# Kernel tuning notes

Measured on AMD Instinct MI355X. Metric: run time of the kernel, lower is better.

The kernel has to match this reference:

```python
import jax, jax.numpy as jnp
import numpy as np
from jax import lax


def _layernorm(x, g, b, eps=1e-5):
    m = x.mean(-1, keepdims=True)
    v = ((x - m) ** 2).mean(-1, keepdims=True)
    return (x - m) * lax.rsqrt(v + eps) * g + b


def _conv1d(x, w, b):
    # x: (B, T, Cin), w: (K, Cin, Cout) -> SAME padding (kernel=3, pad=1)
    y = lax.conv_general_dilated(x, w, (1,), 'SAME',
                                 dimension_numbers=('NWC', 'WIO', 'NWC'))
    return y + b


def _predictor(x, params, mask):
    w1, b1, g1, be1, w2, b2, g2, be2, wl, bl = params
    h = _layernorm(jax.nn.relu(_conv1d(x, w1, b1)), g1, be1)
    h = _layernorm(jax.nn.relu(_conv1d(h, w2, b2)), g2, be2)
    out = (h @ wl)[..., 0] + bl[0]          # (B, T)
    return jnp.where(mask, 0.0, out)


def _length_regulate(x, dur, max_len):
    # vectorized equivalent of the per-token expand/cat/pad loop
    cum = jnp.cumsum(dur, axis=1)            # (B, S)
    mel_len = cum[:, -1]                     # (B,)
    pos = jnp.arange(max_len)                # (T,)
    idx = jax.vmap(lambda c: jnp.searchsorted(c, pos, side='right'))(cum)
    idx = jnp.minimum(idx, x.shape[1] - 1)   # (B, T)
    out = jnp.take_along_axis(x, idx[:, :, None], axis=1)
    valid = (pos[None, :] < mel_len[:, None])[:, :, None]
    return jnp.where(valid, out, 0.0), mel_len


def setup_inputs() -> dict:
    key = jax.random.key(0)
    ks = jax.random.split(key, 12)
    B, S, D, F, K, T, NB = 32, 512, 512, 512, 3, 4096, 256
    inp = {
        'x': jax.random.normal(ks[0], (B, S, D), jnp.float32),
        'src_mask': jnp.zeros((B, S), bool),
        'mel_mask': jnp.zeros((B, T), bool),
        'pitch_truth': jax.random.normal(ks[1], (B, S), jnp.float32),
        'energy_truth': jax.random.normal(ks[2], (B, S), jnp.float32),
        'duration_truth': jax.random.randint(ks[3], (B, S), 0, 8, jnp.int32),
        'conv1_w': 0.05 * jax.random.normal(ks[4], (3, K, D, F), jnp.float32),
        'conv1_b': jnp.zeros((3, F), jnp.float32),
        'ln1_g': jnp.ones((3, F), jnp.float32),
        'ln1_b': jnp.zeros((3, F), jnp.float32),
        'conv2_w': 0.05 * jax.random.normal(ks[5], (3, K, F, F), jnp.float32),
        'conv2_b': jnp.zeros((3, F), jnp.float32),
        'ln2_g': jnp.ones((3, F), jnp.float32),
        'ln2_b': jnp.zeros((3, F), jnp.float32),
        'lin_w': 0.05 * jax.random.normal(ks[6], (3, F, 1), jnp.float32),
        'lin_b': jnp.zeros((3, 1), jnp.float32),
        'pitch_emb': 0.05 * jax.random.normal(ks[7], (NB, D), jnp.float32),
        'energy_emb': 0.05 * jax.random.normal(ks[8], (NB, D), jnp.float32),
        'pitch_bins': jnp.linspace(-3.0, 3.0, NB - 1),
        'energy_bins': jnp.linspace(-3.0, 3.0, NB - 1),
        'max_mel_len': T,
    }
    return inp


def reference(x, src_mask, mel_mask, pitch_truth, energy_truth, duration_truth,
              conv1_w, conv1_b, ln1_g, ln1_b, conv2_w, conv2_b, ln2_g, ln2_b,
              lin_w, lin_b, pitch_emb, energy_emb, pitch_bins, energy_bins,
              max_mel_len):
    def params(i):
        return (conv1_w[i], conv1_b[i], ln1_g[i], ln1_b[i],
                conv2_w[i], conv2_b[i], ln2_g[i], ln2_b[i], lin_w[i], lin_b[i])

    # pitch (predictor idx 0)
    pitch_pred = _predictor(x, params(0), src_mask)
    x = x + pitch_emb[jnp.searchsorted(pitch_bins, pitch_truth, side='left')]
    # energy (idx 1)
    energy_pred = _predictor(x, params(1), src_mask)
    x = x + energy_emb[jnp.searchsorted(energy_bins, energy_truth, side='left')]
    # duration (idx 2)
    log_dur = _predictor(x, params(2), src_mask)
    # length regulation with ground-truth durations (training path)
    x_out, mel_len = _length_regulate(x, duration_truth, max_mel_len)
    return x_out, pitch_pred, energy_pred, log_dur, mel_len, mel_mask
```

## Files before the change

kernel.cpp:

```cpp
#include <hip/hip_runtime.h>
#include <hip/hip_bf16.h>


#define B_ 32
#define S_ 512
#define D_ 512
#define F_ 512
#define T_ 4096
#define SP_ 514
#define KK_ 1536
#define NKT 48
#define SLOT ((size_t)B_ * SP_ * D_)

typedef __attribute__((ext_vector_type(8))) short bf16x8;
typedef __attribute__((ext_vector_type(4))) float f32x4;

__device__ __forceinline__ float bf2f(unsigned short u) {
  union { unsigned int i; float f; } c; c.i = (unsigned int)u << 16; return c.f;
}
__device__ __forceinline__ unsigned short f2bf(float f) {
  __hip_bfloat16 h = __float2bfloat16(f);
  return *(unsigned short*)&h;
}

struct Job {
  const __hip_bfloat16* Pin;
  const __hip_bfloat16* WT;
  const float* bias;
  const float* g;
  const float* be;
  const float* wl;
  const float* bl;
  const unsigned char* mask;
  __hip_bfloat16* Pout;
  float* pred;
  int mode;
};

#define WT_BLKS 1152
#define TP_BLKS 8224
__global__ __launch_bounds__(256) void prep_k(const float* __restrict__ x,
                                              const float* __restrict__ W1,
                                              const float* __restrict__ W2,
                                              const int* __restrict__ dur,
                                              const float* __restrict__ ptruth,
                                              const float* __restrict__ pbins,
                                              const float* __restrict__ pemb,
                                              const float* __restrict__ etruth,
                                              const float* __restrict__ ebins,
                                              const float* __restrict__ eemb,
                                              __hip_bfloat16* __restrict__ X0,
                                              __hip_bfloat16* __restrict__ X1,
                                              __hip_bfloat16* __restrict__ X2,
                                              __hip_bfloat16* __restrict__ P0,
                                              __hip_bfloat16* __restrict__ P1,
                                              __hip_bfloat16* __restrict__ WT1,
                                              __hip_bfloat16* __restrict__ WT2,
                                              int* __restrict__ cum,
                                              float* __restrict__ mel_len) {
  const int blk = blockIdx.x;
  const int t = threadIdx.x;
  if (blk < WT_BLKS) {
    __shared__ float tb[64][65];
    const int w = blk / 192;
    const int kt = (blk % 192) >> 3;
    const int ft = blk & 7;
    const float* src = (w < 3) ? (W1 + (size_t)w * KK_ * F_)
                               : (W2 + (size_t)(w - 3) * KK_ * F_);
    __hip_bfloat16* dst = (w < 3) ? (WT1 + (size_t)w * KK_ * F_)
                                  : (WT2 + (size_t)(w - 3) * KK_ * F_);
    const int ty = t >> 4, tx = t & 15;
    #pragma unroll
    for (int j = 0; j < 4; ++j) {
      const int r = ty + j * 16;
      const float4 v = *(const float4*)(src + (size_t)(kt * 64 + r) * F_ + ft * 64 + tx * 4);
      tb[r][tx * 4 + 0] = v.x; tb[r][tx * 4 + 1] = v.y;
      tb[r][tx * 4 + 2] = v.z; tb[r][tx * 4 + 3] = v.w;
    }
    __syncthreads();
    #pragma unroll
    for (int j = 0; j < 4; ++j) {
      const int r = ty + j * 16;
      ushort4 u = make_ushort4(f2bf(tb[tx * 4 + 0][r]), f2bf(tb[tx * 4 + 1][r]),
                               f2bf(tb[tx * 4 + 2][r]), f2bf(tb[tx * 4 + 3][r]));
      *(ushort4*)((unsigned short*)dst + (size_t)(ft * 64 + r) * KK_ + kt * 64 + tx * 4) = u;
    }
  } else if (blk < WT_BLKS + TP_BLKS) {
    __shared__ int i1s[2], i2s[2];
    const int half = t >> 7;
    const int tl = t & 127;
    const int task = (blk - WT_BLKS) * 2 + half;
    if (task < B_ * S_) {
      if (tl == 0) {
        float v = ptruth[task];
        int lo = 0, hi = 255;
        while (lo < hi) { const int mid = (lo + hi) >> 1; if (pbins[mid] < v) lo = mid + 1; else hi = mid; }
        i1s[half] = lo;
        v = etruth[task]; lo = 0; hi = 255;
        while (lo < hi) { const int mid = (lo + hi) >> 1; if (ebins[mid] < v) lo = mid + 1; else hi = mid; }
        i2s[half] = lo;
      }
      __syncthreads();
      const int b = task >> 9, s = task & 511;
      const size_t off = ((size_t)b * SP_ + s + 1) * D_ + tl * 4;
      const float4 v = *(const float4*)(x + (size_t)task * D_ + tl * 4);
      const float4 pe = *(const float4*)(pemb + (size_t)i1s[half] * D_ + tl * 4);
      const float4 ee = *(const float4*)(eemb + (size_t)i2s[half] * D_ + tl * 4);
      *(ushort4*)((unsigned short*)X0 + off) =
          make_ushort4(f2bf(v.x), f2bf(v.y), f2bf(v.z), f2bf(v.w));
      const float4 v1 = make_float4(v.x + pe.x, v.y + pe.y, v.z + pe.z, v.w + pe.w);
      *(ushort4*)((unsigned short*)X1 + off) =
          make_ushort4(f2bf(v1.x), f2bf(v1.y), f2bf(v1.z), f2bf(v1.w));
      *(ushort4*)((unsigned short*)X2 + off) =
          make_ushort4(f2bf(v1.x + ee.x), f2bf(v1.y + ee.y),
                       f2bf(v1.z + ee.z), f2bf(v1.w + ee.w));
    } else {
      __syncthreads();
      const int idx = task - B_ * S_;
      const int b = idx >> 1;
      const int r = (idx & 1) ? (SP_ - 1) : 0;
      const size_t off = ((size_t)b * SP_ + r) * D_ + tl * 4;
      const ushort4 z = make_ushort4(0, 0, 0, 0);
      *(ushort4*)((unsigned short*)X0 + off) = z;
      *(ushort4*)((unsigned short*)X1 + off) = z;
      *(ushort4*)((unsigned short*)X2 + off) = z;
      *(ushort4*)((unsigned short*)P0 + off) = z;
      *(ushort4*)((unsigned short*)P1 + off) = z;
    }
  } else {
    __shared__ int sh[S_];
    const int b = blk - (WT_BLKS + TP_BLKS);
    sh[t] = dur[b * S_ + t];
    sh[t + 256] = dur[b * S_ + t + 256];
    __syncthreads();
    for (int off = 1; off < S_; off <<= 1) {
      const int a1 = (t >= off) ? sh[t - off] : 0;
      const int j2 = t + 256;
      const int a2 = (j2 >= off) ? sh[j2 - off] : 0;
      __syncthreads();
      sh[t] += a1; sh[j2] += a2;
      __syncthreads();
    }
    cum[b * S_ + t] = sh[t];
    cum[b * S_ + t + 256] = sh[t + 256];
    if (t == 255) mel_len[b] = (float)sh[S_ - 1];
  }
}

__global__ __launch_bounds__(512, 4) void convfuse_k(Job j0, Job j1, Job j2) {
  extern __shared__ char smem[];
  char* As = smem;
  char* Bs = smem + 2 * 4096;
  const int pid = blockIdx.x >> 8;
  const Job jb = (pid == 0) ? j0 : (pid == 1 ? j1 : j2);
  const int inner = blockIdx.x & 255;
  const int swz = (inner & 7) * 32 + (inner >> 3);
  const int b  = swz >> 3;
  const int st = (swz & 7) * 64;
  const int t = threadIdx.x;
  const int lane = t & 63;
  const int wave = t >> 6;
  const int wn = wave * 64;

  f32x4 acc[4][4];
  #pragma unroll
  for (int m = 0; m < 4; ++m)
    #pragma unroll
    for (int n = 0; n < 4; ++n) acc[m][n] = (f32x4){0.f, 0.f, 0.f, 0.f};

  const __hip_bfloat16* Xb = jb.Pin + (size_t)b * SP_ * D_;
  const __hip_bfloat16* WT = jb.WT;

  auto stage = [&](int kt, int buf) {
    char* Ad = As + buf * 4096;
    if (t < 256) {
      const int row = t >> 2, ch = t & 3;
      const __hip_bfloat16* ga = Xb + (size_t)(st + (kt >> 4) + row) * D_ +
                                 (kt & 15) * 32 + (ch ^ ((row >> 1) & 3)) * 8;
      __builtin_amdgcn_global_load_lds(
          (const __attribute__((address_space(1))) void*)ga,
          (__attribute__((address_space(3))) void*)(Ad + t * 16), 16, 0, 0);
    }
    char* Bd = Bs + buf * 32768;
    #pragma unroll
    for (int i = 0; i < 4; ++i) {
      const int c = t + i * 512;
      const int fr = c >> 2, ch = c & 3;
      const __hip_bfloat16* gb = WT + (size_t)fr * KK_ + kt * 32 +
                                 (ch ^ ((fr >> 1) & 3)) * 8;
      __builtin_amdgcn_global_load_lds(
          (const __attribute__((address_space(1))) void*)gb,
          (__attribute__((address_space(3))) void*)(Bd + c * 16), 16, 0, 0);
    }
  };

  stage(0, 0);
  __syncthreads();
  const int rA = lane & 15;
  const int offx = ((lane >> 4) * 16) ^ (((rA >> 1) & 3) << 4);

  for (int kt = 0; kt < NKT; ++kt) {
    const int cur = kt & 1;
    if (kt < NKT - 1) stage(kt + 1, cur ^ 1);
    const char* Ab = As + cur * 4096;
    const char* Bb = Bs + cur * 32768;
    bf16x8 af[4], bf[4];
    #pragma unroll
    for (int m = 0; m < 4; ++m)
      af[m] = *(const bf16x8*)(Ab + (m * 16 + rA) * 64 + offx);
    #pragma unroll
    for (int n = 0; n < 4; ++n)
      bf[n] = *(const bf16x8*)(Bb + (wn + n * 16 + rA) * 64 + offx);
    __builtin_amdgcn_s_setprio(1);
    #pragma unroll
    for (int m = 0; m < 4; ++m)
      #pragma unroll
      for (int n = 0; n < 4; ++n)
        acc[m][n] = __builtin_amdgcn_mfma_f32_16x16x32_bf16(af[m], bf[n], acc[m][n], 0, 0, 0);
    __builtin_amdgcn_s_setprio(0);
    __syncthreads();
  }

  float* rS = (float*)smem;
  float* rQ = rS + 512;
  float* rP = rQ + 512;
  float* tS = rP + 512;
  float* tQ = tS + 64;
  float* tP = tQ + 64;
  float* wG = tP + 64;
  float* wB = wG + 8;

  const int MODE = jb.mode;
  float bia[4], gg[4], bb[4], ww[4];
  #pragma unroll
  for (int n = 0; n < 4; ++n) {
    const int f = wn + n * 16 + rA;
    bia[n] = jb.bias[f]; gg[n] = jb.g[f]; bb[n] = jb.be[f];
    ww[n] = (MODE == 1) ? jb.wl[f] : 0.f;
  }
  if (MODE == 1) {
    float gwp = 0.f, bwp = 0.f;
    #pragma unroll
    for (int n = 0; n < 4; ++n) { gwp += gg[n] * ww[n]; bwp += bb[n] * ww[n]; }
    #pragma unroll
    for (int o = 1; o < 16; o <<= 1) {
      gwp += __shfl_xor(gwp, o); bwp += __shfl_xor(bwp, o);
    }
    if (lane == 0) { wG[wave] = gwp; wB[wave] = bwp; }
  }
  #pragma unroll
  for (int m = 0; m < 4; ++m) {
    #pragma unroll
    for (int r = 0; r < 4; ++r) {
      float sv = 0.f, sq = 0.f, sp = 0.f;
      #pragma unroll
      for (int n = 0; n < 4; ++n) {
        float v = fmaxf(acc[m][n][r] + bia[n], 0.f);
        acc[m][n][r] = v;
        sv += v; sq += v * v;
        sp += v * gg[n] * ww[n];
      }
      #pragma unroll
      for (int o = 1; o < 16; o <<= 1) {
        sv += __shfl_xor(sv, o); sq += __shfl_xor(sq, o);
        sp += __shfl_xor(sp, o);
      }
      if (rA == 0) {
        const int row = m * 16 + (lane >> 4) * 4 + r;
        rS[wave * 64 + row] = sv; rQ[wave * 64 + row] = sq;
        rP[wave * 64 + row] = sp;
      }
    }
  }
  __syncthreads();
  if (t < 64) {
    float S = 0.f, Q = 0.f, Pp = 0.f;
    #pragma unroll
    for (int w = 0; w < 8; ++w) {
      S += rS[w * 64 + t]; Q += rQ[w * 64 + t]; Pp += rP[w * 64 + t];
    }
    tS[t] = S; tQ[t] = Q; tP[t] = Pp;
  }
  __syncthreads();
  if (MODE == 0) {
    unsigned short* Pu = (unsigned short*)jb.Pout;
    #pragma unroll
    for (int m = 0; m < 4; ++m) {
      #pragma unroll
      for (int r = 0; r < 4; ++r) {
        const int row = m * 16 + (lane >> 4) * 4 + r;
        const float mean = tS[row] * (1.f / F_);
        const float var = tQ[row] * (1.f / F_) - mean * mean;
        const float inv = rsqrtf(var + 1e-5f);
        unsigned short* pp =
            Pu + ((size_t)b * SP_ + st + row + 1) * D_ + wn + rA;
        #pragma unroll
        for (int n = 0; n < 4; ++n)
          pp[n * 16] = f2bf((acc[m][n][r] - mean) * inv * gg[n] + bb[n]);
      }
    }
  } else {
    if (t < 64) {
      float GW = 0.f, BW = 0.f;
      #pragma unroll
      for (int w = 0; w < 8; ++w) { GW += wG[w]; BW += wB[w]; }
      const float mean = tS[t] * (1.f / F_);
      const float var = tQ[t] * (1.f / F_) - mean * mean;
      const float inv = rsqrtf(var + 1e-5f);
      const int grow = b * S_ + st + t;
      jb.pred[grow] = jb.mask[grow] ? 0.f
                                    : (inv * tP[t] - inv * mean * GW + BW + jb.bl[0]);
    }
  }
}

__global__ __launch_bounds__(256) void gather_k(const __hip_bfloat16* __restrict__ X,
                                                const int* __restrict__ cum,
                                                const unsigned char* __restrict__ melm,
                                                float* __restrict__ out,
                                                float* __restrict__ maskf) {
  const int b    = blockIdx.x >> 11;
  const int pos0 = (blockIdx.x & 2047) * 2;
  const int half = threadIdx.x >> 7;
  const int tl   = threadIdx.x & 127;
  const int pos  = pos0 + half;
  __shared__ int sidx[2], svalid[2];
  if (tl == 0) {
    const int* c = cum + b * S_;
    int lo = 0, hi = S_;
    while (lo < hi) {
      const int mid = (lo + hi) >> 1;
      if (c[mid] <= pos) lo = mid + 1; else hi = mid;
    }
    sidx[half] = (lo < S_ - 1) ? lo : (S_ - 1);
    svalid[half] = (pos < c[S_ - 1]) ? 1 : 0;
    maskf[(size_t)b * T_ + pos] = melm[(size_t)b * T_ + pos] ? 1.f : 0.f;
  }
  __syncthreads();
  float4 v = make_float4(0.f, 0.f, 0.f, 0.f);
  if (svalid[half]) {
    const ushort4 u = *(const ushort4*)((const unsigned short*)X +
                        ((size_t)b * SP_ + sidx[half] + 1) * D_ + tl * 4);
    v = make_float4(bf2f(u.x), bf2f(u.y), bf2f(u.z), bf2f(u.w));
  }
  *(float4*)(out + ((size_t)b * T_ + pos) * D_ + tl * 4) = v;
}

extern "C" void kernel_launch(void* const* d_in, const int* in_sizes, int n_in,
                              void* d_out, int out_size, void* d_ws, size_t ws_size,
                              hipStream_t stream) {
  const float* x            = (const float*)d_in[0];
  const unsigned char* srcm = (const unsigned char*)d_in[1];
  const unsigned char* melm = (const unsigned char*)d_in[2];
  const float* pitch_truth  = (const float*)d_in[3];
  const float* energy_truth = (const float*)d_in[4];
  const int*   dur          = (const int*)d_in[5];
  const float* conv1_w = (const float*)d_in[6];
  const float* conv1_b = (const float*)d_in[7];
  const float* ln1_g   = (const float*)d_in[8];
  const float* ln1_b   = (const float*)d_in[9];
  const float* conv2_w = (const float*)d_in[10];
  const float* conv2_b = (const float*)d_in[11];
  const float* ln2_g   = (const float*)d_in[12];
  const float* ln2_b   = (const float*)d_in[13];
  const float* lin_w   = (const float*)d_in[14];
  const float* lin_b   = (const float*)d_in[15];
  const float* pitch_emb   = (const float*)d_in[16];
  const float* energy_emb  = (const float*)d_in[17];
  const float* pitch_bins  = (const float*)d_in[18];
  const float* energy_bins = (const float*)d_in[19];

  float* out      = (float*)d_out;
  float* x_out    = out;
  float* p_pitch  = out + (size_t)B_ * T_ * D_;
  float* p_energy = p_pitch + B_ * S_;
  float* p_dur    = p_energy + B_ * S_;
  float* p_mellen = p_dur + B_ * S_;
  float* p_mask   = p_mellen + B_;

  __hip_bfloat16* S0  = (__hip_bfloat16*)d_ws;
  __hip_bfloat16* S1  = S0 + SLOT;
  __hip_bfloat16* S2  = S1 + SLOT;
  __hip_bfloat16* S3  = S2 + SLOT;
  __hip_bfloat16* S4  = S3 + SLOT;
  __hip_bfloat16* WT1 = S4 + SLOT;
  __hip_bfloat16* WT2 = WT1 + (size_t)3 * F_ * KK_;
  int*  cum = (int*)(WT2 + (size_t)3 * F_ * KK_);

  const dim3 blk512t(512), blk256(256);
  const int convLds = 2 * (4096 + 32768);
  hipFuncSetAttribute((const void*)convfuse_k,
                      hipFuncAttributeMaxDynamicSharedMemorySize, convLds);

  prep_k<<<dim3(WT_BLKS + TP_BLKS + B_), blk256, 0, stream>>>(
      x, conv1_w, conv2_w, dur, pitch_truth, pitch_bins, pitch_emb,
      energy_truth, energy_bins, energy_emb,
      S0, S1, S2, S3, S4, WT1, WT2, cum, p_mellen);

  auto c1 = [&](int i, const __hip_bfloat16* in, __hip_bfloat16* Pout) {
    return Job{in, WT1 + (size_t)i * F_ * KK_, conv1_b + (size_t)i * F_,
               ln1_g + (size_t)i * F_, ln1_b + (size_t)i * F_,
               nullptr, nullptr, nullptr, Pout, nullptr, 0};
  };
  auto c2 = [&](int i, const __hip_bfloat16* in, float* pred) {
    return Job{in, WT2 + (size_t)i * F_ * KK_, conv2_b + (size_t)i * F_,
               ln2_g + (size_t)i * F_, ln2_b + (size_t)i * F_,
               lin_w + (size_t)i * F_, lin_b + i, srcm, nullptr, pred, 1};
  };

  {
    Job a = c1(0, S0, S3), b = c1(1, S1, S4);
    convfuse_k<<<dim3(512), blk512t, convLds, stream>>>(a, b, b);
  }
  {
    Job a = c2(0, S3, p_pitch), b = c2(1, S4, p_energy), c = c1(2, S2, S0);
    convfuse_k<<<dim3(768), blk512t, convLds, stream>>>(a, b, c);
  }
  {
    Job a = c2(2, S0, p_dur);
    convfuse_k<<<dim3(256), blk512t, convLds, stream>>>(a, a, a);
  }

  gather_k<<<dim3(B_ * T_ / 2), blk256, 0, stream>>>(S2, cum, melm, x_out, p_mask);
}
```

Measured before the change: 379.3 us.

## Enlarge conv GEMM tile to 128x512 with 8-phase pipelined K loop

Replaces the 64-row by 512-column conv tile with a 128x512 tile split into quadrant phases. Each phase overlaps global-to-LDS loads of the next K slice with MFMA on the current one, using explicit vmcnt waits and barriers. It also rebalances the three launches so each runs two jobs of 128 blocks. The goal is more reuse of the weight tile per block and fewer synchronizations. In exchange, the 160KB LDS footprint and larger accumulator set lower occupancy, and with 256 blocks per launch there may be fewer blocks than CUs would like.

```diff
diff --git a/kernel.cpp b/kernel.cpp
--- a/kernel.cpp
+++ b/kernel.cpp
@@ -9,7 +9,7 @@
 #define T_ 4096
 #define SP_ 514
 #define KK_ 1536
-#define NKT 48
+#define NITER 12
 #define SLOT ((size_t)B_ * SP_ * D_)
 
 typedef __attribute__((ext_vector_type(8))) short bf16x8;
@@ -147,137 +147,181 @@
   }
 }
 
-__global__ __launch_bounds__(512, 4) void convfuse_k(Job j0, Job j1, Job j2) {
+#define GLOAD(gptr, loff) __builtin_amdgcn_global_load_lds(                    \
+    (const __attribute__((address_space(1))) void*)(gptr),                     \
+    (__attribute__((address_space(3))) void*)(smem + (loff)), 16, 0, 0)
+
+#define PHASE(D, AH, BH, STAGE_STMT, VM_STMT)                                  \
+  {                                                                            \
+    bf16x8 aR[2][2], bR[2][4];                                                 \
+    const char* Ab = smem + (D) * 16384 + (AH) * 8192;                         \
+    const char* Bb = smem + 32768 + (D) * 65536 + (BH) * 32768;                \
+    _Pragma("unroll")                                                          \
+    for (int kh = 0; kh < 2; ++kh) {                                           \
+      _Pragma("unroll")                                                        \
+      for (int mi = 0; mi < 2; ++mi) {                                         \
+        const int row = rowbase + 16 * mi;                                     \
+        aR[kh][mi] = *(const bf16x8*)(Ab + row * 128 +                         \
+                                      (((kh * 4 + l4) ^ (row & 7)) * 16));     \
+      }                                                                        \
+      _Pragma("unroll")                                                        \
+      for (int ni = 0; ni < 4; ++ni) {                                         \
+        const int cl = colbase + 16 * ni;                                      \
+        bR[kh][ni] = *(const bf16x8*)(Bb + cl * 128 +                          \
+                                      (((kh * 4 + l4) ^ (cl & 7)) * 16));      \
+      }                                                                        \
+    }                                                                          \
+    STAGE_STMT;                                                                \
+    __builtin_amdgcn_s_barrier();                                              \
+    asm volatile("s_waitcnt lgkmcnt(0)" ::: "memory");                         \
+    __builtin_amdgcn_sched_barrier(0);                                         \
+    __builtin_amdgcn_s_setprio(1);                                             \
+    _Pragma("unroll")                                                          \
+    for (int kh = 0; kh < 2; ++kh)                                             \
+      _Pragma("unroll")                                                        \
+      for (int mi = 0; mi < 2; ++mi)                                           \
+        _Pragma("unroll")                                                      \
+        for (int ni = 0; ni < 4; ++ni)                                         \
+          acc[AH][BH][mi][ni] = __builtin_amdgcn_mfma_f32_16x16x32_bf16(       \
+              aR[kh][mi], bR[kh][ni], acc[AH][BH][mi][ni], 0, 0, 0);           \
+    __builtin_amdgcn_s_setprio(0);                                             \
+    __builtin_amdgcn_sched_barrier(0);                                         \
+    VM_STMT;                                                                   \
+    __builtin_amdgcn_s_barrier();                                              \
+  }
+
+__global__ __launch_bounds__(512, 2) void conv8_k(Job j0, Job j1) {
   extern __shared__ char smem[];
-  char* As = smem;
-  char* Bs = smem + 2 * 4096;
-  const int pid = blockIdx.x >> 8;
-  const Job jb = (pid == 0) ? j0 : (pid == 1 ? j1 : j2);
-  const int inner = blockIdx.x & 255;
-  const int swz = (inner & 7) * 32 + (inner >> 3);
-  const int b  = swz >> 3;
-  const int st = (swz & 7) * 64;
+  const Job jb = (blockIdx.x >> 7) ? j1 : j0;
+  const int inner = blockIdx.x & 127;
+  const int swz = (inner & 7) * 16 + (inner >> 3);
+  const int b  = swz >> 2;
+  const int st = (swz & 3) * 128;
   const int t = threadIdx.x;
   const int lane = t & 63;
   const int wave = t >> 6;
-  const int wn = wave * 64;
-
-  f32x4 acc[4][4];
+  const int wm2 = wave >> 2;
+  const int wn  = wave & 3;
+  const int rA = lane & 15;
+  const int l4 = lane >> 4;
+  const int rowbase = 32 * wm2 + rA;
+  const int colbase = 64 * wn + rA;
+
+  f32x4 acc[2][2][2][4];
   #pragma unroll
-  for (int m = 0; m < 4; ++m)
-    #pragma unroll
-    for (int n = 0; n < 4; ++n) acc[m][n] = (f32x4){0.f, 0.f, 0.f, 0.f};
-
-  const __hip_bfloat16* Xb = jb.Pin + (size_t)b * SP_ * D_;
-  const __hip_bfloat16* WT = jb.WT;
-
-  auto stage = [&](int kt, int buf) {
-    char* Ad = As + buf * 4096;
-    if (t < 256) {
-      const int row = t >> 2, ch = t & 3;
-      const __hip_bfloat16* ga = Xb + (size_t)(st + (kt >> 4) + row) * D_ +
-                                 (kt & 15) * 32 + (ch ^ ((row >> 1) & 3)) * 8;
-      __builtin_amdgcn_global_load_lds(
-          (const __attribute__((address_space(1))) void*)ga,
-          (__attribute__((address_space(3))) void*)(Ad + t * 16), 16, 0, 0);
-    }
-    char* Bd = Bs + buf * 32768;
+  for (int a = 0; a < 2; ++a)
+    #pragma unroll
+    for (int c = 0; c < 2; ++c)
+      #pragma unroll
+      for (int m = 0; m < 2; ++m)
+        #pragma unroll
+        for (int n = 0; n < 4; ++n) acc[a][c][m][n] = (f32x4){0.f, 0.f, 0.f, 0.f};
+
+  auto stageA = [&](int kt, int half) {
+    const int r = t >> 3, ch = t & 7;
+    const __hip_bfloat16* ga = jb.Pin +
+        ((size_t)b * SP_ + st + half * 64 + r + (kt >> 3)) * D_ +
+        (kt & 7) * 64 + (ch ^ (r & 7)) * 8;
+    GLOAD(ga, (kt & 1) * 16384 + half * 8192 + t * 16);
+  };
+  auto stageB = [&](int kt, int half) {
     #pragma unroll
     for (int i = 0; i < 4; ++i) {
       const int c = t + i * 512;
-      const int fr = c >> 2, ch = c & 3;
-      const __hip_bfloat16* gb = WT + (size_t)fr * KK_ + kt * 32 +
-                                 (ch ^ ((fr >> 1) & 3)) * 8;
-      __builtin_amdgcn_global_load_lds(
-          (const __attribute__((address_space(1))) void*)gb,
-          (__attribute__((address_space(3))) void*)(Bd + c * 16), 16, 0, 0);
+      const int fr = c >> 3, ch = c & 7;
+      const __hip_bfloat16* gb = jb.WT +
+          (size_t)(half * 256 + fr) * KK_ + kt * 64 + (ch ^ (fr & 7)) * 8;
+      GLOAD(gb, 32768 + (kt & 1) * 65536 + half * 32768 + c * 16);
     }
   };
 
-  stage(0, 0);
-  __syncthreads();
-  const int rA = lane & 15;
-  const int offx = ((lane >> 4) * 16) ^ (((rA >> 1) & 3) << 4);
-
-  for (int kt = 0; kt < NKT; ++kt) {
-    const int cur = kt & 1;
-    if (kt < NKT - 1) stage(kt + 1, cur ^ 1);
-    const char* Ab = As + cur * 4096;
-    const char* Bb = Bs + cur * 32768;
-    bf16x8 af[4], bf[4];
-    #pragma unroll
-    for (int m = 0; m < 4; ++m)
-      af[m] = *(const bf16x8*)(Ab + (m * 16 + rA) * 64 + offx);
-    #pragma unroll
-    for (int n = 0; n < 4; ++n)
-      bf[n] = *(const bf16x8*)(Bb + (wn + n * 16 + rA) * 64 + offx);
-    __builtin_amdgcn_s_setprio(1);
-    #pragma unroll
-    for (int m = 0; m < 4; ++m)
-      #pragma unroll
-      for (int n = 0; n < 4; ++n)
-        acc[m][n] = __builtin_amdgcn_mfma_f32_16x16x32_bf16(af[m], bf[n], acc[m][n], 0, 0, 0);
-    __builtin_amdgcn_s_setprio(0);
-    __syncthreads();
+  stageA(0, 0); stageB(0, 0); stageA(0, 1); stageB(0, 1);
+  stageA(1, 0); stageB(1, 1);
+  asm volatile("s_waitcnt vmcnt(5)" ::: "memory");
+  __builtin_amdgcn_s_barrier();
+
+  for (int it = 0; it < NITER; ++it) {
+    const int tk = 2 * it;
+    const bool more = (it < NITER - 1);
+    PHASE(0, 0, 0, { stageB(tk + 1, 0); }, );
+    PHASE(0, 0, 1, { stageA(tk + 1, 1); }, );
+    PHASE(0, 1, 1, { if (more) stageA(tk + 2, 0); }, );
+    PHASE(0, 1, 0, { if (more) stageB(tk + 2, 1); },
+          if (more) { asm volatile("s_waitcnt vmcnt(5)" ::: "memory"); }
+          else      { asm volatile("s_waitcnt vmcnt(0)" ::: "memory"); });
+    PHASE(1, 0, 0, { if (more) stageB(tk + 2, 0); }, );
+    PHASE(1, 0, 1, { if (more) stageA(tk + 2, 1); }, );
+    PHASE(1, 1, 1, { if (more) stageA(tk + 3, 0); }, );
+    PHASE(1, 1, 0, { if (more) stageB(tk + 3, 1); },
+          if (more) { asm volatile("s_waitcnt vmcnt(5)" ::: "memory"); }
+          else      { asm volatile("s_waitcnt vmcnt(0)" ::: "memory"); });
   }
 
   float* rS = (float*)smem;
   float* rQ = rS + 512;
   float* rP = rQ + 512;
   float* tS = rP + 512;
-  float* tQ = tS + 64;
-  float* tP = tQ + 64;
-  float* wG = tP + 64;
-  float* wB = wG + 8;
+  float* tQ = tS + 128;
+  float* tP = tQ + 128;
+  float* wG = tP + 128;
+  float* wB = wG + 4;
 
   const int MODE = jb.mode;
-  float bia[4], gg[4], bb[4], ww[4];
+  float bia[2][4], gg[2][4], bb[2][4], ww[2][4];
   #pragma unroll
-  for (int n = 0; n < 4; ++n) {
-    const int f = wn + n * 16 + rA;
-    bia[n] = jb.bias[f]; gg[n] = jb.g[f]; bb[n] = jb.be[f];
-    ww[n] = (MODE == 1) ? jb.wl[f] : 0.f;
-  }
-  if (MODE == 1) {
+  for (int bh = 0; bh < 2; ++bh)
+    #pragma unroll
+    for (int ni = 0; ni < 4; ++ni) {
+      const int f = 64 * wn + bh * 256 + 16 * ni + rA;
+      bia[bh][ni] = jb.bias[f]; gg[bh][ni] = jb.g[f]; bb[bh][ni] = jb.be[f];
+      ww[bh][ni] = (MODE == 1) ? jb.wl[f] : 0.f;
+    }
+  if (MODE == 1 && wm2 == 0) {
     float gwp = 0.f, bwp = 0.f;
     #pragma unroll
-    for (int n = 0; n < 4; ++n) { gwp += gg[n] * ww[n]; bwp += bb[n] * ww[n]; }
+    for (int bh = 0; bh < 2; ++bh)
+      #pragma unroll
+      for (int ni = 0; ni < 4; ++ni) {
+        gwp += gg[bh][ni] * ww[bh][ni]; bwp += bb[bh][ni] * ww[bh][ni];
+      }
     #pragma unroll
     for (int o = 1; o < 16; o <<= 1) {
       gwp += __shfl_xor(gwp, o); bwp += __shfl_xor(bwp, o);
     }
-    if (lane == 0) { wG[wave] = gwp; wB[wave] = bwp; }
+    if (lane == 0) { wG[wn] = gwp; wB[wn] = bwp; }
   }
   #pragma unroll
-  for (int m = 0; m < 4; ++m) {
-    #pragma unroll
-    for (int r = 0; r < 4; ++r) {
-      float sv = 0.f, sq = 0.f, sp = 0.f;
+  for (int ah = 0; ah < 2; ++ah)
+    #pragma unroll
+    for (int mi = 0; mi < 2; ++mi)
       #pragma unroll
-      for (int n = 0; n < 4; ++n) {
-        float v = fmaxf(acc[m][n][r] + bia[n], 0.f);
-        acc[m][n][r] = v;
-        sv += v; sq += v * v;
-        sp += v * gg[n] * ww[n];
+      for (int reg = 0; reg < 4; ++reg) {
+        float sv = 0.f, sq = 0.f, sp = 0.f;
+        #pragma unroll
+        for (int bh = 0; bh < 2; ++bh)
+          #pragma unroll
+          for (int ni = 0; ni < 4; ++ni) {
+            float v = fmaxf(acc[ah][bh][mi][ni][reg] + bia[bh][ni], 0.f);
+            acc[ah][bh][mi][ni][reg] = v;
+            sv += v; sq += v * v;
+            sp += v * gg[bh][ni] * ww[bh][ni];
+          }
+        #pragma unroll
+        for (int o = 1; o < 16; o <<= 1) {
+          sv += __shfl_xor(sv, o); sq += __shfl_xor(sq, o);
+          sp += __shfl_xor(sp, o);
+        }
+        if (rA == 0) {
+          const int lr = 64 * ah + 32 * wm2 + 16 * mi + l4 * 4 + reg;
+          rS[wn * 128 + lr] = sv; rQ[wn * 128 + lr] = sq; rP[wn * 128 + lr] = sp;
+        }
       }
-      #pragma unroll
-      for (int o = 1; o < 16; o <<= 1) {
-        sv += __shfl_xor(sv, o); sq += __shfl_xor(sq, o);
-        sp += __shfl_xor(sp, o);
-      }
-      if (rA == 0) {
-        const int row = m * 16 + (lane >> 4) * 4 + r;
-        rS[wave * 64 + row] = sv; rQ[wave * 64 + row] = sq;
-        rP[wave * 64 + row] = sp;
-      }
-    }
-  }
   __syncthreads();
-  if (t < 64) {
+  if (t < 128) {
     float S = 0.f, Q = 0.f, Pp = 0.f;
     #pragma unroll
-    for (int w = 0; w < 8; ++w) {
-      S += rS[w * 64 + t]; Q += rQ[w * 64 + t]; Pp += rP[w * 64 + t];
+    for (int w = 0; w < 4; ++w) {
+      S += rS[w * 128 + t]; Q += rQ[w * 128 + t]; Pp += rP[w * 128 + t];
     }
     tS[t] = S; tQ[t] = Q; tP[t] = Pp;
   }
@@ -285,25 +329,27 @@
   if (MODE == 0) {
     unsigned short* Pu = (unsigned short*)jb.Pout;
     #pragma unroll
-    for (int m = 0; m < 4; ++m) {
+    for (int ah = 0; ah < 2; ++ah)
       #pragma unroll
-      for (int r = 0; r < 4; ++r) {
-        const int row = m * 16 + (lane >> 4) * 4 + r;
-        const float mean = tS[row] * (1.f / F_);
-        const float var = tQ[row] * (1.f / F_) - mean * mean;
-        const float inv = rsqrtf(var + 1e-5f);
-        unsigned short* pp =
-            Pu + ((size_t)b * SP_ + st + row + 1) * D_ + wn + rA;
+      for (int mi = 0; mi < 2; ++mi)
         #pragma unroll
-        for (int n = 0; n < 4; ++n)
-          pp[n * 16] = f2bf((acc[m][n][r] - mean) * inv * gg[n] + bb[n]);
-      }
-    }
+        for (int reg = 0; reg < 4; ++reg) {
+          const int lr = 64 * ah + 32 * wm2 + 16 * mi + l4 * 4 + reg;
+          const float mean = tS[lr] * (1.f / F_);
+          const float var = tQ[lr] * (1.f / F_) - mean * mean;
+          const float inv = rsqrtf(var + 1e-5f);
+          unsigned short* pp = Pu + ((size_t)b * SP_ + st + lr + 1) * D_;
+          #pragma unroll
+          for (int bh = 0; bh < 2; ++bh)
+            #pragma unroll
+            for (int ni = 0; ni < 4; ++ni)
+              pp[64 * wn + bh * 256 + 16 * ni + rA] =
+                  f2bf((acc[ah][bh][mi][ni][reg] - mean) * inv * gg[bh][ni] + bb[bh][ni]);
+        }
   } else {
-    if (t < 64) {
-      float GW = 0.f, BW = 0.f;
-      #pragma unroll
-      for (int w = 0; w < 8; ++w) { GW += wG[w]; BW += wB[w]; }
+    if (t < 128) {
+      const float GW = wG[0] + wG[1] + wG[2] + wG[3];
+      const float BW = wB[0] + wB[1] + wB[2] + wB[3];
       const float mean = tS[t] * (1.f / F_);
       const float var = tQ[t] * (1.f / F_) - mean * mean;
       const float inv = rsqrtf(var + 1e-5f);
@@ -388,8 +434,8 @@
   int*  cum = (int*)(WT2 + (size_t)3 * F_ * KK_);
 
   const dim3 blk512t(512), blk256(256);
-  const int convLds = 2 * (4096 + 32768);
-  hipFuncSetAttribute((const void*)convfuse_k,
+  const int convLds = 163840;
+  hipFuncSetAttribute((const void*)conv8_k,
                       hipFuncAttributeMaxDynamicSharedMemorySize, convLds);
 
   prep_k<<<dim3(WT_BLKS + TP_BLKS + B_), blk256, 0, stream>>>(
@@ -410,15 +456,15 @@
 
   {
     Job a = c1(0, S0, S3), b = c1(1, S1, S4);
-    convfuse_k<<<dim3(512), blk512t, convLds, stream>>>(a, b, b);
+    conv8_k<<<dim3(256), blk512t, convLds, stream>>>(a, b);
   }
   {
-    Job a = c2(0, S3, p_pitch), b = c2(1, S4, p_energy), c = c1(2, S2, S0);
-    convfuse_k<<<dim3(768), blk512t, convLds, stream>>>(a, b, c);
+    Job a = c2(0, S3, p_pitch), b = c1(2, S2, S0);
+    conv8_k<<<dim3(256), blk512t, convLds, stream>>>(a, b);
   }
   {
-    Job a = c2(2, S0, p_dur);
-    convfuse_k<<<dim3(256), blk512t, convLds, stream>>>(a, a, a);
+    Job a = c2(1, S4, p_energy), b = c2(2, S0, p_dur);
+    conv8_k<<<dim3(256), blk512t, convLds, stream>>>(a, b);
   }
 
   gather_k<<<dim3(B_ * T_ / 2), blk256, 0, stream>>>(S2, cum, melm, x_out, p_mask);
```

New measurement: 320.2 us. -15.6%, faster.
